# Performance work log

Hardware: AMD Instinct MI355X
Metric: run time of the kernel (lower is better)

## Reference

```python
import jax, jax.numpy as jnp
import numpy as np

T_SEG = 8          # num_segments
L_WIN = 5          # temporal window
S_WIN = 9          # spatial window (window[1] == window[2])


def _conv3d(x, w, p):
    # x: (N, Cin, T, H, W), w: (Cout, Cin, kt, kh, kw), spatial pad p
    return jax.lax.conv_general_dilated(
        x, w, (1, 1, 1), [(0, 0), (p, p), (p, p)],
        dimension_numbers=('NCDHW', 'OIDHW', 'NCDHW'))


def _bn_gelu(x, scale, shift):
    # eval-mode BatchNorm3d folded into per-channel scale/shift, then exact GELU
    s = scale[None, :, None, None, None]
    b = shift[None, :, None, None, None]
    return jax.nn.gelu(x * s + b, approximate=False)


def reference(x, ln_gamma, ln_beta, in_w, in_b,
              ext_w, ext_scale, ext_shift,
              i0_w, i0_scale, i0_shift,
              i1_w, i1_scale, i1_shift,
              i2_w, i2_scale, i2_shift,
              out_w, out_b):
    L, BT, D = x.shape
    H = W = int(np.sqrt(L))
    T = T_SEG
    b = BT // T
    Lw = L_WIN
    U = S_WIN
    m = S_WIN // 2

    # ---- LayerNorm (fp32) + in_proj ----
    xf = x.astype(jnp.float32)
    mu = xf.mean(-1, keepdims=True)
    var = xf.var(-1, keepdims=True)
    xn = (xf - mu) * jax.lax.rsqrt(var + 1e-5) * ln_gamma + ln_beta
    h0 = xn @ in_w.T + in_b                       # (L, BT, DH)
    DH = h0.shape[-1]
    f = h0.reshape(H, W, BT, DH).transpose(2, 3, 0, 1)   # (BT, C, H, W)

    # ---- STSSTransformation ----
    f5 = f.reshape(b, T, DH, H, W)
    f_src = jnp.broadcast_to(f5[:, :, None], (b, T, Lw, DH, H, W)).reshape(-1, DH, H, W)
    fp = jnp.pad(f5, ((0, 0), (Lw // 2, Lw // 2), (0, 0), (0, 0), (0, 0)))
    # unfold over time: x_tgt[b, t, l] = padded[b, t + l]
    f_tgt = jnp.stack([fp[:, i:i + T] for i in range(Lw)], axis=2).reshape(-1, DH, H, W)

    def _n(v):  # F.normalize(p=2, dim=1, eps=1e-7)
        return v / jnp.maximum(jnp.sqrt((v * v).sum(1, keepdims=True)), 1e-7)

    corr = jnp.einsum('bchw,bcuv->bhwuv', _n(f_src), _n(f_tgt))  # (b*T*Lw, H, W, H, W)

    # global -> local: corr_l[b,h,w,u,v] = corr[b,h,w,h+u-m,w+v-m], pad value 0 (cosine)
    cp = jnp.pad(corr, ((0, 0), (0, 0), (0, 0), (m, m), (m, m)))
    hh = jnp.arange(H); ww = jnp.arange(W); dd = jnp.arange(U)
    h_i = hh[:, None, None, None]
    w_i = ww[None, :, None, None]
    u_i = h_i + dd[None, None, :, None]
    v_i = w_i + dd[None, None, None, :]
    corr_l = cp[:, h_i, w_i, u_i, v_i]            # (b*T*Lw, H, W, U, U)

    # 'b t h w 1 l u v -> (b l) (u v) t h w'
    s = (corr_l.reshape(b, T, Lw, H, W, U, U)
               .transpose(0, 2, 5, 6, 1, 3, 4)
               .reshape(b * Lw, U * U, T, H, W))

    # ---- STSSExtraction ----
    y = _bn_gelu(_conv3d(s, ext_w, 0), ext_scale, ext_shift)     # (b*Lw, 64, T, H, W)

    # ---- STSSIntegration ----
    y = _bn_gelu(_conv3d(y, i0_w, 1), i0_scale, i0_shift)
    y = _bn_gelu(_conv3d(y, i1_w, 1), i1_scale, i1_shift)
    C1 = y.shape[1]
    y = y.reshape(b, Lw * C1, T, H, W)            # '(b l) c -> b (l c)'
    y = _bn_gelu(_conv3d(y, i2_w, 1), i2_scale, i2_shift)        # (b, 64, T, H, W)

    # ---- out_proj: 'b c t h w -> (h w) (b t) c' ----
    C2 = y.shape[1]
    y = y.transpose(3, 4, 0, 2, 1).reshape(H * W, b * T, C2)
    return y @ out_w.T + out_b


def setup_inputs() -> dict:
    key = jax.random.key(0)
    ks = jax.random.split(key, 10)
    D, DH, T, B, H, W = 768, 64, 8, 16, 14, 14
    Lw, U = 5, 9
    C = 64
    p = lambda k, shape, s: (jax.random.normal(k, shape, jnp.float32) * s)
    return {
        'x': jax.random.normal(ks[0], (H * W, B * T, D), jnp.float32),
        'ln_gamma': jnp.ones((D,), jnp.float32),
        'ln_beta': jnp.zeros((D,), jnp.float32),
        'in_w': p(ks[1], (DH, D), 0.02),
        'in_b': jnp.zeros((DH,), jnp.float32),
        'ext_w': p(ks[2], (C, U * U, 1, 1, 1), 0.1),
        'ext_scale': jnp.ones((C,), jnp.float32),
        'ext_shift': jnp.zeros((C,), jnp.float32),
        'i0_w': p(ks[3], (C, C, 1, 3, 3), 0.05),
        'i0_scale': jnp.ones((C,), jnp.float32),
        'i0_shift': jnp.zeros((C,), jnp.float32),
        'i1_w': p(ks[4], (C, C, 1, 3, 3), 0.05),
        'i1_scale': jnp.ones((C,), jnp.float32),
        'i1_shift': jnp.zeros((C,), jnp.float32),
        'i2_w': p(ks[5], (C, Lw * C, 1, 3, 3), 0.03),
        'i2_scale': jnp.ones((C,), jnp.float32),
        'i2_shift': jnp.zeros((C,), jnp.float32),
        'out_w': p(ks[6], (D, C), 0.02),
        'out_b': jnp.zeros((D,), jnp.float32),
    }
```

## Files before the change

kernel.cpp:

```cpp
#include <hip/hip_runtime.h>


__device__ __forceinline__ float gelu_exact(float x) {
    return 0.5f * x * (1.0f + erff(x * 0.70710678118654752440f));
}

__global__ void k_prep(const float* __restrict__ in_w, const float* __restrict__ gamma,
                       const float* __restrict__ ext_w, const float* __restrict__ out_w,
                       float* __restrict__ A, float* __restrict__ extT, float* __restrict__ wT) {
    int idx = blockIdx.x * 256 + threadIdx.x;
    if (idx < 64 * 768) {
        int c = idx / 768, d = idx % 768;
        A[idx]  = in_w[idx] * gamma[d];
        wT[idx] = out_w[d * 64 + c];
    }
    if (idx < 81 * 64) {
        int k = idx / 64, co = idx % 64;
        extT[idx] = ext_w[co * 81 + k];
    }
}

__global__ void k_gb(const float* __restrict__ in_w, const float* __restrict__ gamma,
                     const float* __restrict__ beta, const float* __restrict__ in_b,
                     float* __restrict__ Gc, float* __restrict__ Bc) {
    int c = blockIdx.x, tid = threadIdx.x;
    float s1 = 0.f, s2 = 0.f;
    for (int d = tid; d < 768; d += 256) {
        float w = in_w[c * 768 + d];
        s1 += w * gamma[d];
        s2 += w * beta[d];
    }
    __shared__ float r1[256], r2[256];
    r1[tid] = s1; r2[tid] = s2;
    __syncthreads();
    for (int s = 128; s > 0; s >>= 1) {
        if (tid < s) { r1[tid] += r1[tid + s]; r2[tid] += r2[tid + s]; }
        __syncthreads();
    }
    if (tid == 0) { Gc[c] = r1[0]; Bc[c] = r2[0] + in_b[c]; }
}

#define XPITCH(r) ((r) * 68 + ((r) >> 2) * 4)

__global__ __launch_bounds__(128) void k_lnproj(
    const float* __restrict__ x, const float* __restrict__ A,
    const float* __restrict__ Gc, const float* __restrict__ Bc,
    float* __restrict__ fn)
{
    const int l   = blockIdx.x;
    const int bq  = blockIdx.y;
    const int tid = threadIdx.x;

    __shared__ __align__(16) float xs[4416];
    __shared__ __align__(16) float as[4416];
    __shared__ float redA[64][16];
    __shared__ float redB[64][16];
    __shared__ float mu_s[64], rs_s[64], inv_s[64];

    const int btg  = tid >> 3;
    const int cgrp = tid & 7;
    const int b0 = btg * 4, c0 = cgrp * 8;
    const int srow = tid >> 4;
    const int sdq  = tid & 15;

    float acc[4][8] = {};
    float ssum[8] = {}, ssq[8] = {};

#pragma unroll 1
    for (int kc = 0; kc < 12; ++kc) {
#pragma unroll
        for (int k = 0; k < 8; ++k) {
            int r = srow + 8 * k;
            float4 v = *(const float4*)&x[((size_t)(l * 128 + bq * 64 + r)) * 768 + kc * 64 + sdq * 4];
            *(float4*)&xs[XPITCH(r) + sdq * 4] = v;
            ssum[k] += v.x + v.y + v.z + v.w;
            ssq[k]  += v.x * v.x + v.y * v.y + v.z * v.z + v.w * v.w;
        }
#pragma unroll
        for (int k = 0; k < 8; ++k) {
            int c = srow + 8 * k;
            float4 v = *(const float4*)&A[(size_t)c * 768 + kc * 64 + sdq * 4];
            *(float4*)&as[XPITCH(c) + sdq * 4] = v;
        }
        __syncthreads();
#pragma unroll 4
        for (int dq = 0; dq < 16; ++dq) {
            float4 xv[4], av[8];
#pragma unroll
            for (int i = 0; i < 4; ++i)
                xv[i] = *(const float4*)&xs[XPITCH(b0 + i) + dq * 4];
#pragma unroll
            for (int j = 0; j < 8; ++j)
                av[j] = *(const float4*)&as[XPITCH(c0 + j) + dq * 4];
#pragma unroll
            for (int i = 0; i < 4; ++i)
#pragma unroll
                for (int j = 0; j < 8; ++j)
                    acc[i][j] += xv[i].x * av[j].x + xv[i].y * av[j].y +
                                 xv[i].z * av[j].z + xv[i].w * av[j].w;
        }
        __syncthreads();
    }

#pragma unroll
    for (int k = 0; k < 8; ++k) {
        redA[srow + 8 * k][sdq] = ssum[k];
        redB[srow + 8 * k][sdq] = ssq[k];
    }
    __syncthreads();
    if (tid < 64) {
        float s1 = 0.f, s2 = 0.f;
        for (int q = 0; q < 16; ++q) { s1 += redA[tid][q]; s2 += redB[tid][q]; }
        float mu  = s1 * (1.f / 768.f);
        float var = s2 * (1.f / 768.f) - mu * mu;
        mu_s[tid] = mu;
        rs_s[tid] = rsqrtf(var + 1e-5f);
    }
    __syncthreads();

    float h0v[4][8];
#pragma unroll
    for (int i = 0; i < 4; ++i) {
        float mu = mu_s[b0 + i], rs = rs_s[b0 + i];
        float ns = 0.f;
#pragma unroll
        for (int j = 0; j < 8; ++j) {
            float a = rs * acc[i][j] - mu * rs * Gc[c0 + j] + Bc[c0 + j];
            h0v[i][j] = a;
            ns += a * a;
        }
        redA[b0 + i][cgrp] = ns;
    }
    __syncthreads();
    if (tid < 64) {
        float s = 0.f;
        for (int q = 0; q < 8; ++q) s += redA[tid][q];
        inv_s[tid] = 1.f / fmaxf(sqrtf(s), 1e-7f);
    }
    __syncthreads();
#pragma unroll
    for (int i = 0; i < 4; ++i) {
        float inv = inv_s[b0 + i];
        int bt = bq * 64 + b0 + i;
        float4 v0 = make_float4(h0v[i][0] * inv, h0v[i][1] * inv, h0v[i][2] * inv, h0v[i][3] * inv);
        float4 v1 = make_float4(h0v[i][4] * inv, h0v[i][5] * inv, h0v[i][6] * inv, h0v[i][7] * inv);
        *(float4*)&fn[((size_t)bt * 196 + l) * 64 + c0] = v0;
        *(float4*)&fn[((size_t)bt * 196 + l) * 64 + c0 + 4] = v1;
    }
}

__global__ __launch_bounds__(256) void k_corr_ext(
    const float* __restrict__ fn, const float* __restrict__ extT,
    const float* __restrict__ e_scale, const float* __restrict__ e_shift,
    float* __restrict__ y0)
{
    extern __shared__ float smem[];
    float* srcT = smem;
    float* tgtT = smem + 952;
    float* csum = smem + 14416;

    const int h   = blockIdx.x;
    const int n   = blockIdx.y;
    const int l   = n % 5, t = (n / 5) % 8, b = n / 40;
    const int tid = threadIdx.x;
    const int bt  = b * 8 + t;
    const int tt  = t + l - 2;
    const bool tval = (tt >= 0) && (tt < 8);
    const int bt2 = b * 8 + (tval ? tt : 0);

    for (int i4 = tid; i4 < 14 * 16; i4 += 256) {
        int w = i4 >> 4, c4 = i4 & 15;
        *(float4*)&srcT[w * 68 + c4 * 4] =
            *(const float4*)&fn[((size_t)bt * 196 + h * 14 + w) * 64 + c4 * 4];
    }
    for (int i4 = tid; i4 < 9 * 22 * 16; i4 += 256) {
        int du = i4 / (22 * 16), r = i4 % (22 * 16);
        int xx = r >> 4, c4 = r & 15;
        int row = h + du - 4, xc = xx - 4;
        float4 v = make_float4(0.f, 0.f, 0.f, 0.f);
        if (tval && row >= 0 && row < 14 && xc >= 0 && xc < 14)
            v = *(const float4*)&fn[((size_t)bt2 * 196 + row * 14 + xc) * 64 + c4 * 4];
        *(float4*)&tgtT[(du * 22 + xx) * 68 + c4 * 4] = v;
    }
    __syncthreads();

    if (tid < 252) {
        int item = tid >> 1, ch = tid & 1;
        int w = item / 9, du = item % 9;
        float acc[9] = {};
        int row = h + du - 4;
        if (tval && row >= 0 && row < 14) {
            const float* sp = &srcT[w * 68 + ch * 32];
            const float* tp = &tgtT[du * 22 * 68 + ch * 32];
            for (int cq = 0; cq < 8; ++cq) {
                float4 s4 = *(const float4*)&sp[cq * 4];
#pragma unroll
                for (int dv = 0; dv < 9; ++dv) {
                    float4 t4 = *(const float4*)&tp[(w + dv) * 68 + cq * 4];
                    acc[dv] += s4.x * t4.x + s4.y * t4.y + s4.z * t4.z + s4.w * t4.w;
                }
            }
        }
#pragma unroll
        for (int dv = 0; dv < 9; ++dv)
            acc[dv] += __shfl_xor(acc[dv], 1);
        if (ch == 0) {
#pragma unroll
            for (int dv = 0; dv < 9; ++dv)
                csum[w * 84 + du * 9 + dv] = acc[dv];
        }
    }
    __syncthreads();

    if (tid < 224) {
        const int w = tid % 14, cg = tid / 14;
        const int co0 = cg * 4;
        const float* cp = &csum[w * 84];
        float a0 = 0.f, a1 = 0.f, a2 = 0.f, a3 = 0.f;
#pragma unroll 3
        for (int k = 0; k < 81; ++k) {
            float s = cp[k];
            float4 e = *(const float4*)&extT[k * 64 + co0];
            a0 = fmaf(s, e.x, a0);
            a1 = fmaf(s, e.y, a1);
            a2 = fmaf(s, e.z, a2);
            a3 = fmaf(s, e.w, a3);
        }
        const size_t obase = ((size_t)(b * 5 + l) * 64) * 1568 + (size_t)t * 196 + h * 14;
        float r[4] = {a0, a1, a2, a3};
#pragma unroll
        for (int j = 0; j < 4; ++j) {
            float v = gelu_exact(r[j] * e_scale[co0 + j] + e_shift[co0 + j]);
            y0[obase + (size_t)(co0 + j) * 1568 + w] = v;
        }
    }
}

__global__ __launch_bounds__(256) void k_conv3x3(
    const float* __restrict__ in, const float* __restrict__ w,
    const float* __restrict__ scale, const float* __restrict__ shift,
    float* __restrict__ out, int CT, int bn)
{
    extern __shared__ float smem[];
    float* inp = smem;

    const int t   = blockIdx.x;
    const int nb  = blockIdx.y;
    const int z   = blockIdx.z;
    const int tid = threadIdx.x;
    const int CIN9 = CT * 64 * 9;

    for (int i = tid; i < (64 * 288) / 2; i += 256)
        ((float2*)inp)[i] = make_float2(0.f, 0.f);
    __syncthreads();
    const size_t ibase = ((size_t)(nb * CT + z) * 64) * 1568 + (size_t)t * 196;
    for (int i = tid; i < 64 * 196; i += 256) {
        int ci = i / 196, pos = i % 196;
        int hh = pos / 14, ww = pos % 14;
        inp[ci * 288 + (hh + 1) * 18 + (ww + 1)] = in[ibase + (size_t)ci * 1568 + pos];
    }
    __syncthreads();

    float acc[4][14] = {};
    const int cg = tid / 14, hr = tid % 14;
    const int co0 = cg * 4;
    if (tid < 224) {
        for (int ci = 0; ci < 64; ++ci) {
            float r[3][16];
#pragma unroll
            for (int kh = 0; kh < 3; ++kh)
#pragma unroll
                for (int k2 = 0; k2 < 8; ++k2)
                    *(float2*)&r[kh][k2 * 2] =
                        *(const float2*)&inp[ci * 288 + (hr + kh) * 18 + k2 * 2];
            const float* wp = &w[(size_t)(z * 64 + ci) * 9];
#pragma unroll
            for (int kh = 0; kh < 3; ++kh)
#pragma unroll
                for (int kw = 0; kw < 3; ++kw) {
                    float wv[4];
#pragma unroll
                    for (int j = 0; j < 4; ++j)
                        wv[j] = wp[(size_t)(co0 + j) * CIN9 + kh * 3 + kw];
#pragma unroll
                    for (int j = 0; j < 4; ++j)
#pragma unroll
                        for (int q = 0; q < 14; ++q)
                            acc[j][q] = fmaf(r[kh][q + kw], wv[j], acc[j][q]);
                }
        }
        if (bn) {
#pragma unroll
            for (int j = 0; j < 4; ++j) {
                int co = co0 + j;
                float sc = scale[co], sh = shift[co];
                size_t ob = (size_t)(nb * 64 + co) * 1568 + (size_t)t * 196 + hr * 14;
#pragma unroll
                for (int q = 0; q < 14; ++q)
                    out[ob + q] = gelu_exact(acc[j][q] * sc + sh);
            }
        } else {
#pragma unroll
            for (int j = 0; j < 4; ++j) {
                int co = co0 + j;
                size_t ob = ((size_t)(z * gridDim.y + nb) * 64 + co) * 1568 + (size_t)t * 196 + hr * 14;
#pragma unroll
                for (int q = 0; q < 14; ++q)
                    out[ob + q] = acc[j][q];
            }
        }
    }
}

__global__ void k_sum_bn(const float* __restrict__ yp, const float* __restrict__ scale,
                         const float* __restrict__ shift, float* __restrict__ y3) {
    int idx = blockIdx.x * 256 + threadIdx.x;
    if (idx >= 16 * 64 * 8 * 196) return;
    float s = 0.f;
#pragma unroll
    for (int z = 0; z < 5; ++z) s += yp[(size_t)z * 1605632 + idx];
    int co = (idx / 1568) & 63;
    y3[idx] = gelu_exact(s * scale[co] + shift[co]);
}

__global__ __launch_bounds__(192) void k_out(
    const float* __restrict__ y3, const float* __restrict__ wT,
    const float* __restrict__ out_b, float* __restrict__ out)
{
    const int l   = blockIdx.x;
    const int bg  = blockIdx.y;
    const int tid = threadIdx.x;
    __shared__ __align__(16) float ysB[8][64];
    for (int i = tid; i < 512; i += 192) {
        int bl = i >> 6, c = i & 63;
        int bt = bg * 8 + bl;
        ysB[bl][c] = y3[((size_t)((bt >> 3) * 64 + c) * 8 + (bt & 7)) * 196 + l];
    }
    __syncthreads();
    const int d0 = tid * 4;
    float acc[8][4] = {};
    for (int cq = 0; cq < 16; ++cq) {
        float4 ys[8];
#pragma unroll
        for (int i = 0; i < 8; ++i) ys[i] = *(const float4*)&ysB[i][cq * 4];
#pragma unroll
        for (int cc = 0; cc < 4; ++cc) {
            float4 wv = *(const float4*)&wT[(size_t)(cq * 4 + cc) * 768 + d0];
#pragma unroll
            for (int i = 0; i < 8; ++i) {
                float yv = (cc == 0) ? ys[i].x : (cc == 1) ? ys[i].y : (cc == 2) ? ys[i].z : ys[i].w;
                acc[i][0] = fmaf(yv, wv.x, acc[i][0]);
                acc[i][1] = fmaf(yv, wv.y, acc[i][1]);
                acc[i][2] = fmaf(yv, wv.z, acc[i][2]);
                acc[i][3] = fmaf(yv, wv.w, acc[i][3]);
            }
        }
    }
    float4 ob = *(const float4*)&out_b[d0];
#pragma unroll
    for (int i = 0; i < 8; ++i) {
        float4 v = make_float4(acc[i][0] + ob.x, acc[i][1] + ob.y,
                               acc[i][2] + ob.z, acc[i][3] + ob.w);
        *(float4*)&out[((size_t)(l * 128 + bg * 8 + i)) * 768 + d0] = v;
    }
}

extern "C" void kernel_launch(void* const* d_in, const int* in_sizes, int n_in,
                              void* d_out, int out_size, void* d_ws, size_t ws_size,
                              hipStream_t stream) {
    const float* x         = (const float*)d_in[0];
    const float* ln_gamma  = (const float*)d_in[1];
    const float* ln_beta   = (const float*)d_in[2];
    const float* in_w      = (const float*)d_in[3];
    const float* in_b      = (const float*)d_in[4];
    const float* ext_w     = (const float*)d_in[5];
    const float* ext_scale = (const float*)d_in[6];
    const float* ext_shift = (const float*)d_in[7];
    const float* i0_w      = (const float*)d_in[8];
    const float* i0_scale  = (const float*)d_in[9];
    const float* i0_shift  = (const float*)d_in[10];
    const float* i1_w      = (const float*)d_in[11];
    const float* i1_scale  = (const float*)d_in[12];
    const float* i1_shift  = (const float*)d_in[13];
    const float* i2_w      = (const float*)d_in[14];
    const float* i2_scale  = (const float*)d_in[15];
    const float* i2_shift  = (const float*)d_in[16];
    const float* out_w     = (const float*)d_in[17];
    const float* out_b     = (const float*)d_in[18];

    float* ws   = (float*)d_ws;
    float* A    = ws;
    float* Gc   = ws + 49152;
    float* Bc   = ws + 49216;
    float* extT = ws + 49280;
    float* wT   = ws + 54464;
    float* fn   = ws + 103616;
    float* bufA = ws + 1709248;
    float* y3   = ws + 8131776;
    float* outf = (float*)d_out;

    k_prep<<<192, 256, 0, stream>>>(in_w, ln_gamma, ext_w, out_w, A, extT, wT);
    k_gb<<<64, 256, 0, stream>>>(in_w, ln_gamma, ln_beta, in_b, Gc, Bc);
    k_lnproj<<<dim3(196, 2), 128, 0, stream>>>(x, A, Gc, Bc, fn);
    k_corr_ext<<<dim3(14, 640), 256, 62368, stream>>>(fn, extT, ext_scale, ext_shift, bufA);
    k_conv3x3<<<dim3(8, 80, 1), 256, 73728, stream>>>(bufA, i0_w, i0_scale, i0_shift, outf, 1, 1);
    k_conv3x3<<<dim3(8, 80, 1), 256, 73728, stream>>>(outf, i1_w, i1_scale, i1_shift, bufA, 1, 1);
    k_conv3x3<<<dim3(8, 16, 5), 256, 73728, stream>>>(bufA, i2_w, nullptr, nullptr, outf, 5, 0);
    k_sum_bn<<<6272, 256, 0, stream>>>(outf, i2_scale, i2_shift, y3);
    k_out<<<dim3(196, 16), 192, 0, stream>>>(y3, wT, out_b, outf);
}
```

Before: 925.4 us.

## Restructure correlation kernel: channel-split staging, register tiling over w, DPP reduction

The correlation/extraction kernel now stages source and target features in two 32-channel halves. This roughly halves shared memory and allows a 4-blocks-per-SM launch bound with static LDS. Each thread group computes a 5×9 register tile of correlations, reusing each target load across five source positions, and reduces across 8 channel lanes with DPP moves instead of shuffles. The extraction matvec also reads csum as float4. This raises register pressure from 45 accumulators per thread and leaves a number of threads idle.

```diff
diff --git a/kernel.cpp b/kernel.cpp
--- a/kernel.cpp
+++ b/kernel.cpp
@@ -4,6 +4,9 @@
 __device__ __forceinline__ float gelu_exact(float x) {
     return 0.5f * x * (1.0f + erff(x * 0.70710678118654752440f));
 }
+
+#define DPP_ADD(v, CTRL) \
+    ((v) + __int_as_float(__builtin_amdgcn_mov_dpp(__float_as_int(v), (CTRL), 0xF, 0xF, true)))
 
 __global__ void k_prep(const float* __restrict__ in_w, const float* __restrict__ gamma,
                        const float* __restrict__ ext_w, const float* __restrict__ out_w,
@@ -149,15 +152,15 @@
     }
 }
 
-__global__ __launch_bounds__(256) void k_corr_ext(
+__global__ __launch_bounds__(256, 4) void k_corr_ext(
     const float* __restrict__ fn, const float* __restrict__ extT,
     const float* __restrict__ e_scale, const float* __restrict__ e_shift,
     float* __restrict__ y0)
 {
-    extern __shared__ float smem[];
+    __shared__ __align__(16) float smem[8808];
     float* srcT = smem;
-    float* tgtT = smem + 952;
-    float* csum = smem + 14416;
+    float* tgtT = smem + 504;
+    float* csum = smem + 7632;
 
     const int h   = blockIdx.x;
     const int n   = blockIdx.y;
@@ -168,46 +171,78 @@
     const bool tval = (tt >= 0) && (tt < 8);
     const int bt2 = b * 8 + (tval ? tt : 0);
 
-    for (int i4 = tid; i4 < 14 * 16; i4 += 256) {
-        int w = i4 >> 4, c4 = i4 & 15;
-        *(float4*)&srcT[w * 68 + c4 * 4] =
-            *(const float4*)&fn[((size_t)bt * 196 + h * 14 + w) * 64 + c4 * 4];
-    }
-    for (int i4 = tid; i4 < 9 * 22 * 16; i4 += 256) {
-        int du = i4 / (22 * 16), r = i4 % (22 * 16);
-        int xx = r >> 4, c4 = r & 15;
-        int row = h + du - 4, xc = xx - 4;
-        float4 v = make_float4(0.f, 0.f, 0.f, 0.f);
-        if (tval && row >= 0 && row < 14 && xc >= 0 && xc < 14)
-            v = *(const float4*)&fn[((size_t)bt2 * 196 + row * 14 + xc) * 64 + c4 * 4];
-        *(float4*)&tgtT[(du * 22 + xx) * 68 + c4 * 4] = v;
-    }
-    __syncthreads();
-
-    if (tid < 252) {
-        int item = tid >> 1, ch = tid & 1;
-        int w = item / 9, du = item % 9;
-        float acc[9] = {};
-        int row = h + du - 4;
-        if (tval && row >= 0 && row < 14) {
-            const float* sp = &srcT[w * 68 + ch * 32];
-            const float* tp = &tgtT[du * 22 * 68 + ch * 32];
-            for (int cq = 0; cq < 8; ++cq) {
-                float4 s4 = *(const float4*)&sp[cq * 4];
-#pragma unroll
-                for (int dv = 0; dv < 9; ++dv) {
-                    float4 t4 = *(const float4*)&tp[(w + dv) * 68 + cq * 4];
-                    acc[dv] += s4.x * t4.x + s4.y * t4.y + s4.z * t4.z + s4.w * t4.w;
+    const int item = tid >> 3;
+    const int ch   = tid & 7;
+    const int du   = item % 9;
+    const int wg   = item / 9;
+    const int w0   = wg * 5;
+    const int row  = h + du - 4;
+    const bool rvalid = tval && (row >= 0) && (row < 14) && (item < 27);
+
+    float acc[5][9] = {};
+
+#pragma unroll 1
+    for (int s = 0; s < 2; ++s) {
+        const int cb = s * 32;
+        if (tid < 112) {
+            int w = tid >> 3, c4 = tid & 7;
+            *(float4*)&srcT[w * 36 + c4 * 4] =
+                *(const float4*)&fn[((size_t)bt * 196 + h * 14 + w) * 64 + cb + c4 * 4];
+        }
+        for (int i4 = tid; i4 < 9 * 22 * 8; i4 += 256) {
+            int c4 = i4 & 7, rest = i4 >> 3;
+            int xx = rest % 22, r = rest / 22;
+            int grow = h + r - 4, xc = xx - 4;
+            float4 v = make_float4(0.f, 0.f, 0.f, 0.f);
+            if (tval && grow >= 0 && grow < 14 && xc >= 0 && xc < 14)
+                v = *(const float4*)&fn[((size_t)bt2 * 196 + grow * 14 + xc) * 64 + cb + c4 * 4];
+            *(float4*)&tgtT[rest * 36 + c4 * 4] = v;
+        }
+        __syncthreads();
+
+        if (rvalid) {
+            const float* tp = &tgtT[(du * 22) * 36 + ch * 4];
+            float4 sv[5];
+#pragma unroll
+            for (int wi = 0; wi < 5; ++wi) {
+                int w = w0 + wi;
+                sv[wi] = (w < 14) ? *(const float4*)&srcT[w * 36 + ch * 4]
+                                  : make_float4(0.f, 0.f, 0.f, 0.f);
+            }
+#pragma unroll
+            for (int xi = 0; xi < 13; ++xi) {
+                float4 t4 = *(const float4*)&tp[(w0 + xi) * 36];
+#pragma unroll
+                for (int wi = 0; wi < 5; ++wi) {
+                    int dv = xi - wi;
+                    if (dv >= 0 && dv < 9)
+                        acc[wi][dv] += sv[wi].x * t4.x + sv[wi].y * t4.y +
+                                       sv[wi].z * t4.z + sv[wi].w * t4.w;
                 }
             }
         }
-#pragma unroll
-        for (int dv = 0; dv < 9; ++dv)
-            acc[dv] += __shfl_xor(acc[dv], 1);
-        if (ch == 0) {
-#pragma unroll
-            for (int dv = 0; dv < 9; ++dv)
-                csum[w * 84 + du * 9 + dv] = acc[dv];
+        __syncthreads();
+    }
+
+#pragma unroll
+    for (int wi = 0; wi < 5; ++wi)
+#pragma unroll
+        for (int dv = 0; dv < 9; ++dv) {
+            float v = acc[wi][dv];
+            v = DPP_ADD(v, 0xB1);
+            v = DPP_ADD(v, 0x4E);
+            v = DPP_ADD(v, 0x141);
+            acc[wi][dv] = v;
+        }
+    if (ch == 0 && item < 27) {
+#pragma unroll
+        for (int wi = 0; wi < 5; ++wi) {
+            int w = w0 + wi;
+            if (w < 14) {
+#pragma unroll
+                for (int dv = 0; dv < 9; ++dv)
+                    csum[w * 84 + du * 9 + dv] = acc[wi][dv];
+            }
         }
     }
     __syncthreads();
@@ -217,15 +252,27 @@
         const int co0 = cg * 4;
         const float* cp = &csum[w * 84];
         float a0 = 0.f, a1 = 0.f, a2 = 0.f, a3 = 0.f;
-#pragma unroll 3
-        for (int k = 0; k < 81; ++k) {
-            float s = cp[k];
-            float4 e = *(const float4*)&extT[k * 64 + co0];
-            a0 = fmaf(s, e.x, a0);
-            a1 = fmaf(s, e.y, a1);
-            a2 = fmaf(s, e.z, a2);
-            a3 = fmaf(s, e.w, a3);
-        }
+#pragma unroll 4
+        for (int j = 0; j < 20; ++j) {
+            float4 cs = *(const float4*)&cp[j * 4];
+            float4 e0 = *(const float4*)&extT[(j * 4 + 0) * 64 + co0];
+            float4 e1 = *(const float4*)&extT[(j * 4 + 1) * 64 + co0];
+            float4 e2 = *(const float4*)&extT[(j * 4 + 2) * 64 + co0];
+            float4 e3 = *(const float4*)&extT[(j * 4 + 3) * 64 + co0];
+            a0 = fmaf(cs.x, e0.x, a0); a1 = fmaf(cs.x, e0.y, a1);
+            a2 = fmaf(cs.x, e0.z, a2); a3 = fmaf(cs.x, e0.w, a3);
+            a0 = fmaf(cs.y, e1.x, a0); a1 = fmaf(cs.y, e1.y, a1);
+            a2 = fmaf(cs.y, e1.z, a2); a3 = fmaf(cs.y, e1.w, a3);
+            a0 = fmaf(cs.z, e2.x, a0); a1 = fmaf(cs.z, e2.y, a1);
+            a2 = fmaf(cs.z, e2.z, a2); a3 = fmaf(cs.z, e2.w, a3);
+            a0 = fmaf(cs.w, e3.x, a0); a1 = fmaf(cs.w, e3.y, a1);
+            a2 = fmaf(cs.w, e3.z, a2); a3 = fmaf(cs.w, e3.w, a3);
+        }
+        float c80 = cp[80];
+        float4 e = *(const float4*)&extT[80 * 64 + co0];
+        a0 = fmaf(c80, e.x, a0); a1 = fmaf(c80, e.y, a1);
+        a2 = fmaf(c80, e.z, a2); a3 = fmaf(c80, e.w, a3);
+
         const size_t obase = ((size_t)(b * 5 + l) * 64) * 1568 + (size_t)t * 196 + h * 14;
         float r[4] = {a0, a1, a2, a3};
 #pragma unroll
@@ -402,7 +449,7 @@
     k_prep<<<192, 256, 0, stream>>>(in_w, ln_gamma, ext_w, out_w, A, extT, wT);
     k_gb<<<64, 256, 0, stream>>>(in_w, ln_gamma, ln_beta, in_b, Gc, Bc);
     k_lnproj<<<dim3(196, 2), 128, 0, stream>>>(x, A, Gc, Bc, fn);
-    k_corr_ext<<<dim3(14, 640), 256, 62368, stream>>>(fn, extT, ext_scale, ext_shift, bufA);
+    k_corr_ext<<<dim3(14, 640), 256, 0, stream>>>(fn, extT, ext_scale, ext_shift, bufA);
     k_conv3x3<<<dim3(8, 80, 1), 256, 73728, stream>>>(bufA, i0_w, i0_scale, i0_shift, outf, 1, 1);
     k_conv3x3<<<dim3(8, 80, 1), 256, 73728, stream>>>(outf, i1_w, i1_scale, i1_shift, bufA, 1, 1);
     k_conv3x3<<<dim3(8, 16, 5), 256, 73728, stream>>>(bufA, i2_w, nullptr, nullptr, outf, 5, 0);
```

Measured after the change: 906.7 us. 2.0% less time.
